# Kernel tuning notes

Hardware: AMD Instinct MI355X
Metric: run time of the kernel (lower is better)

Reference implementation:

```python
import jax, jax.numpy as jnp
import numpy as np

K = 32        # neighbors kept
SCALE = 1     # dilation stride for dilated kNN


def setup_inputs() -> dict:
    key = jax.random.key(0)
    ks = jax.random.split(key, 8)
    s = 0.05  # weight init scale
    return {
        "x": jax.random.normal(ks[0], (16, 3, 4096), jnp.float32),
        "w1": jax.random.normal(ks[1], (64, 3), jnp.float32) * s,
        "b1": jnp.zeros((64,), jnp.float32),
        "w2": jax.random.normal(ks[2], (128, 64), jnp.float32) * s,
        "b2": jnp.zeros((128,), jnp.float32),
        "w3": jax.random.normal(ks[3], (1024, 128), jnp.float32) * s,
        "b3": jnp.zeros((1024,), jnp.float32),
        "fw1": jax.random.normal(ks[4], (512, 1024), jnp.float32) * s,
        "fb1": jnp.zeros((512,), jnp.float32),
        "fw2": jax.random.normal(ks[5], (256, 512), jnp.float32) * s,
        "fb2": jnp.zeros((256,), jnp.float32),
        "fw3": jax.random.normal(ks[6], (9, 256), jnp.float32) * s,
        "fb3": jnp.zeros((9,), jnp.float32),
    }


def _knn_idx(x):
    # x: (B, C, N). Returns (B, N, K) indices of K nearest neighbors (dilated by SCALE).
    inner = jnp.einsum('bcn,bcm->bnm', x, x)            # (B, N, N)
    sq = jnp.sum(x * x, axis=1)                          # (B, N)
    neg_dist = 2.0 * inner - sq[:, :, None] - sq[:, None, :]  # = -||xi-xj||^2
    _, idx = jax.lax.top_k(neg_dist, K * SCALE)          # (B, N, K*SCALE)
    return idx[:, :, ::SCALE]                            # (B, N, K)


def reference(x, w1, b1, w2, b2, w3, b3, fw1, fb1, fw2, fb2, fw3, fb3):
    B, C, N = x.shape
    idx = _knn_idx(x)                                    # (B, N, K)
    xt = jnp.swapaxes(x, 1, 2)                           # (B, N, C)
    # gather neighbors: nbrs[b,n,k,c] = xt[b, idx[b,n,k], c]
    nbrs = jax.vmap(lambda xb, ib: xb[ib])(xt, idx)      # (B, N, K, C)
    x0 = nbrs - xt[:, :, None, :]                        # edge features x_j - x_i

    # STN (T-Net): shared MLP over edges, global max pool, FC head -> 3x3 transform
    h = jax.nn.relu(jnp.einsum('bnkc,oc->bnko', x0, w1) + b1)
    h = jax.nn.relu(jnp.einsum('bnkc,oc->bnko', h, w2) + b2)
    h = jax.nn.relu(jnp.einsum('bnkc,oc->bnko', h, w3) + b3)
    g = jnp.max(h, axis=(1, 2))                          # (B, 1024)
    f = jax.nn.relu(g @ fw1.T + fb1)
    f = jax.nn.relu(f @ fw2.T + fb2)
    t = (f @ fw3.T + fb3).reshape(B, 3, 3) + jnp.eye(3, dtype=x.dtype)

    out = jnp.einsum('bnc,bcd->bnd', xt, t)              # bmm(x^T, t)
    return jnp.swapaxes(out, 1, 2)                       # (B, 3, N)
```

## Files before the change

### kernel.cpp

```cpp
#include <hip/hip_runtime.h>
#include <hip/hip_fp8.h>

typedef __bf16 bf16_t;
typedef __bf16 bf16x8 __attribute__((ext_vector_type(8)));
typedef float floatx16 __attribute__((ext_vector_type(16)));
typedef int intx8 __attribute__((ext_vector_type(8)));
typedef unsigned long long u64;

#define B_ 16
#define N_ 4096
#define K_ 32


__device__ __forceinline__ unsigned enc_f(float f) {
    unsigned u = __float_as_uint(f);
    return (u & 0x80000000u) ? ~u : (u | 0x80000000u);
}
__device__ __forceinline__ float dec_f(unsigned e) {
    return __uint_as_float((e & 0x80000000u) ? (e & 0x7fffffffu) : ~e);
}

__device__ __forceinline__ void ce(unsigned& a, unsigned& b) {
    const unsigned mn = a < b ? a : b;
    const unsigned mx = a < b ? b : a;
    a = mn; b = mx;
}

__global__ __launch_bounds__(512, 4) void knn_kernel(
    const float* __restrict__ x, const float* __restrict__ w3,
    const float* __restrict__ w2, unsigned short* __restrict__ idxb,
    unsigned* __restrict__ g_enc, unsigned char* __restrict__ w3f8,
    bf16_t* __restrict__ w2sw)
{
    __shared__ __align__(16) float4 cand[16 * 257];
    unsigned* lists = (unsigned*)cand;
    unsigned* m1 = ((unsigned*)cand) + 8192;
    const int tid = threadIdx.x;
    const int bid = blockIdx.x;

    {
        const int g = bid * 512 + tid;
        if (g < 131072) {
            const int j  = g & 31;
            const int lI = (g >> 5) & 63;
            const int kq = (g >> 11) & 1;
            const int cb = g >> 12;
            const int mt2 = kq * 2 + (j >> 4), q = j & 15;
            const int lmI = lI & 31, hiI = lI >> 5;
            const int ch = mt2 * 32 + (q & 3) + 8 * (q >> 2) + 4 * hiI;
            __hip_fp8_e4m3 t(16.0f * w3[(cb * 32 + lmI) * 128 + ch]);
            w3f8[g] = t.__x;
        } else if (g < 139264) {
            const int o = g - 131072;
            const int f = o >> 9, r = o & 511, lI = r >> 3, jj = r & 7;
            const int ks = f & 3, nb = f >> 2, lmI = lI & 31, hiI = lI >> 5;
            w2sw[o] = (bf16_t)w2[(nb * 32 + lmI) * 64 + ks * 16 + hiI * 8 + jj];
        } else if (g < 155648) {
            g_enc[g - 139264] = 0u;
        }
    }

    const int b  = bid >> 7;
    const int q  = tid >> 4;
    const int n  = (bid & 127) * 32 + q;
    const int t  = tid & 15;
    const float* xb = x + b * 3 * N_;

    for (int j = tid; j < N_; j += 512) {
        float cx = xb[j], cy = xb[N_ + j], cz = xb[2 * N_ + j];
        cand[j + (j >> 8)] = make_float4(-2.f * cx, -2.f * cy, -2.f * cz,
                                         fmaf(cx, cx, fmaf(cy, cy, cz * cz)));
    }
    __syncthreads();

    const float xi0 = xb[n], xi1 = xb[N_ + n], xi2 = xb[2 * N_ + n];
    const float xisq1 = fmaf(xi0, xi0, fmaf(xi1, xi1, xi2 * xi2)) + 1.0f;

    unsigned r[8];
    #pragma unroll
    for (int s = 0; s < 8; s++) r[s] = 0x7F7FFFFFu;

    const int j0 = t * 256;
    const int pb = t * 257;
    #pragma unroll 1
    for (int jb = 0; jb < 256; jb += 8) {
        unsigned k[8];
        #pragma unroll
        for (int u = 0; u < 8; u++) {
            const float4 c = cand[pb + jb + u];
            const float d = fmaf(c.z, xi2, fmaf(c.y, xi1, fmaf(c.x, xi0, c.w)));
            k[u] = (__float_as_uint(d + xisq1) & 0xFFFFF000u)
                 | (unsigned)(j0 + jb + u);
        }
        ce(k[0], k[1]); ce(k[2], k[3]); ce(k[4], k[5]); ce(k[6], k[7]);
        ce(k[0], k[2]); ce(k[1], k[3]); ce(k[4], k[6]); ce(k[5], k[7]);
        ce(k[1], k[2]); ce(k[5], k[6]);
        ce(k[0], k[4]); ce(k[1], k[5]); ce(k[2], k[6]); ce(k[3], k[7]);
        ce(k[2], k[4]); ce(k[3], k[5]);
        ce(k[1], k[2]); ce(k[3], k[4]); ce(k[5], k[6]);
        unsigned s[8];
        #pragma unroll
        for (int u = 0; u < 8; u++)
            s[u] = r[u] < k[7 - u] ? r[u] : k[7 - u];
        ce(s[0], s[4]); ce(s[1], s[5]); ce(s[2], s[6]); ce(s[3], s[7]);
        ce(s[0], s[2]); ce(s[1], s[3]); ce(s[4], s[6]); ce(s[5], s[7]);
        ce(s[0], s[1]); ce(s[2], s[3]); ce(s[4], s[5]); ce(s[6], s[7]);
        #pragma unroll
        for (int u = 0; u < 8; u++) r[u] = s[u];
    }
    __syncthreads();

    #pragma unroll
    for (int k = 0; k < 8; k++) lists[tid * 9 + k] = r[k];
    __syncthreads();

    if (tid < 128) {
        const int q1 = tid >> 2, gi = tid & 3;
        const int base = (q1 * 16 + gi * 4) * 9;
        unsigned h0 = lists[base], h1 = lists[base + 9];
        unsigned h2 = lists[base + 18], h3 = lists[base + 27];
        int p0 = 0, p1 = 0, p2 = 0, p3 = 0;
        unsigned* outp = m1 + (q1 * 4 + gi) * 32;
        #pragma unroll 1
        for (int k = 0; k < 32; k++) {
            const unsigned m01 = h0 < h1 ? h0 : h1;
            const unsigned m23 = h2 < h3 ? h2 : h3;
            const unsigned v = m01 < m23 ? m01 : m23;
            outp[k] = v;
            if (m01 < m23) {
                if (h1 < h0) { p1++; h1 = p1 < 8 ? lists[base + 9 + p1] : 0xFFFFFFFFu; }
                else         { p0++; h0 = p0 < 8 ? lists[base + p0]     : 0xFFFFFFFFu; }
            } else {
                if (h3 < h2) { p3++; h3 = p3 < 8 ? lists[base + 27 + p3] : 0xFFFFFFFFu; }
                else         { p2++; h2 = p2 < 8 ? lists[base + 18 + p2] : 0xFFFFFFFFu; }
            }
        }
    }
    __syncthreads();

    if (tid < 32) {
        const unsigned* g0 = m1 + tid * 128;
        unsigned h0 = g0[0], h1 = g0[32], h2 = g0[64], h3 = g0[96];
        int p0 = 0, p1 = 0, p2 = 0, p3 = 0;
        const int nq = (bid & 127) * 32 + tid;
        unsigned short* op = idxb + ((size_t)(b * N_ + nq)) * K_;
        #pragma unroll 1
        for (int k = 0; k < K_; k++) {
            const unsigned m01 = h0 < h1 ? h0 : h1;
            const unsigned m23 = h2 < h3 ? h2 : h3;
            const unsigned v = m01 < m23 ? m01 : m23;
            op[k] = (unsigned short)(v & 0xFFFu);
            if (m01 < m23) {
                if (h1 < h0) { p1++; h1 = p1 < 32 ? g0[32 + p1] : 0xFFFFFFFFu; }
                else         { p0++; h0 = p0 < 32 ? g0[p0]      : 0xFFFFFFFFu; }
            } else {
                if (h3 < h2) { p3++; h3 = p3 < 32 ? g0[96 + p3] : 0xFFFFFFFFu; }
                else         { p2++; h2 = p2 < 32 ? g0[64 + p2] : 0xFFFFFFFFu; }
            }
        }
    }
}

__device__ __forceinline__ void chunk_epilogue(
    const floatx16& a0, const floatx16& a1, int cb, unsigned* gl, int lm)
{
    float c0 = fmaxf(a0[0], a1[0]);
    float c1 = fmaxf(a0[1], a1[1]);
    float c2 = fmaxf(a0[2], a1[2]);
    float c3 = fmaxf(a0[3], a1[3]);
    #pragma unroll
    for (int o = 4; o < 16; o += 4) {
        c0 = fmaxf(fmaxf(a0[o + 0], a1[o + 0]), c0);
        c1 = fmaxf(fmaxf(a0[o + 1], a1[o + 1]), c1);
        c2 = fmaxf(fmaxf(a0[o + 2], a1[o + 2]), c2);
        c3 = fmaxf(fmaxf(a0[o + 3], a1[o + 3]), c3);
    }
    const float m = fmaxf(fmaxf(c0, c1), fmaxf(c2, c3));
    atomicMax(&gl[cb * 32 + lm], enc_f(m));
}

__global__ __launch_bounds__(256, 3) void mlp_kernel(
    const float* __restrict__ x, const unsigned short* __restrict__ idxb,
    const float* __restrict__ w1, const float* __restrict__ b1,
    const float* __restrict__ b2,
    const bf16_t* __restrict__ w2sw, const unsigned char* __restrict__ w3f8,
    unsigned* __restrict__ g_enc)
{
    __shared__ unsigned gl[1024];
    __shared__ __align__(16) float4 w1l[64];
    __shared__ __align__(16) float b2s[128];

    const int tid = threadIdx.x;
    const int b   = blockIdx.x >> 9;
    const int p0  = (blockIdx.x & 511) * 8;
    const float* xb = x + b * 3 * N_;

    const int wv = tid >> 6;
    const int l  = tid & 63;
    const int lm = l & 31;
    const int hi = l >> 5;

    for (int i = tid; i < 1024; i += 256) gl[i] = 0u;
    if (tid < 64)
        w1l[tid] = make_float4(w1[tid * 3], w1[tid * 3 + 1], w1[tid * 3 + 2], b1[tid]);
    else if (tid < 192)
        b2s[tid - 64] = 256.0f * b2[tid - 64];
    __syncthreads();

    const unsigned char* w3p = w3f8 + l * 32;
#define PREFETCH_W3(dst, c) do {                                              \
        dst[0] = *(const intx8*)(w3p + (c) * 4096);                           \
        dst[1] = *(const intx8*)(w3p + (c) * 4096 + 2048);                    \
    } while (0)

    intx8 bwA[2], bwB[2];
    PREFETCH_W3(bwA, 0);

    bf16x8 b1h[2][4];
    float d0[2], d1[2], d2[2];
    #pragma unroll
    for (int nt2 = 0; nt2 < 2; nt2++) {
        const int pp = p0 + wv * 2 + nt2;
        const int j  = idxb[((size_t)(b * N_ + pp)) * K_ + lm];
        d0[nt2] = xb[j]          - xb[pp];
        d1[nt2] = xb[N_ + j]     - xb[N_ + pp];
        d2[nt2] = xb[2 * N_ + j] - xb[2 * N_ + pp];
    }
    #pragma unroll
    for (int ks = 0; ks < 4; ks++)
        #pragma unroll
        for (int jj = 0; jj < 8; jj++) {
            const float4 w = w1l[ks * 16 + hi * 8 + jj];
            #pragma unroll
            for (int nt2 = 0; nt2 < 2; nt2++)
                b1h[nt2][ks][jj] = (bf16_t)fmaxf(
                    fmaf(w.z, d2[nt2], fmaf(w.y, d1[nt2], fmaf(w.x, d0[nt2], w.w))), 0.f);
        }

    intx8 a3v[2][2];
    #pragma unroll
    for (int mt2 = 0; mt2 < 4; mt2++) {
        floatx16 acc0 = (floatx16)0.f, acc1 = (floatx16)0.f;
        #pragma unroll
        for (int ks = 0; ks < 4; ks++) {
            const bf16x8 aw = *(const bf16x8*)&w2sw[((mt2 * 4 + ks) * 64 + l) * 8];
            acc0 = __builtin_amdgcn_mfma_f32_32x32x16_bf16(aw, b1h[0][ks], acc0, 0, 0, 0);
            acc1 = __builtin_amdgcn_mfma_f32_32x32x16_bf16(aw, b1h[1][ks], acc1, 0, 0, 0);
        }
        const int kq = mt2 >> 1, c0 = (mt2 & 1) * 4;
        #pragma unroll
        for (int i2 = 0; i2 < 4; i2++) {
            const float4 bb = *(const float4*)&b2s[mt2 * 32 + i2 * 8 + hi * 4];
            {
                const float v0 = fmaxf(fmaf(acc0[4 * i2 + 0], 256.f, bb.x), 0.f);
                const float v1 = fmaxf(fmaf(acc0[4 * i2 + 1], 256.f, bb.y), 0.f);
                const float v2 = fmaxf(fmaf(acc0[4 * i2 + 2], 256.f, bb.z), 0.f);
                const float v3 = fmaxf(fmaf(acc0[4 * i2 + 3], 256.f, bb.w), 0.f);
                int w = __builtin_amdgcn_cvt_pk_fp8_f32(v0, v1, 0, false);
                w = __builtin_amdgcn_cvt_pk_fp8_f32(v2, v3, w, true);
                a3v[0][kq][c0 + i2] = w;
            }
            {
                const float v0 = fmaxf(fmaf(acc1[4 * i2 + 0], 256.f, bb.x), 0.f);
                const float v1 = fmaxf(fmaf(acc1[4 * i2 + 1], 256.f, bb.y), 0.f);
                const float v2 = fmaxf(fmaf(acc1[4 * i2 + 2], 256.f, bb.z), 0.f);
                const float v3 = fmaxf(fmaf(acc1[4 * i2 + 3], 256.f, bb.w), 0.f);
                int w = __builtin_amdgcn_cvt_pk_fp8_f32(v0, v1, 0, false);
                w = __builtin_amdgcn_cvt_pk_fp8_f32(v2, v3, w, true);
                a3v[1][kq][c0 + i2] = w;
            }
        }
    }

    const floatx16 zf = (floatx16)0.f;

#define COMPUTE_W3(d0_, d1_, buf) do {                                        \
        __builtin_amdgcn_s_setprio(1);                                        \
        d0_ = __builtin_amdgcn_mfma_scale_f32_32x32x64_f8f6f4(                \
            a3v[0][0], buf[0], zf, 0, 0, 0, 0x7F7F7F7F, 0, 0x7F7F7F7F);       \
        d1_ = __builtin_amdgcn_mfma_scale_f32_32x32x64_f8f6f4(                \
            a3v[1][0], buf[0], zf, 0, 0, 0, 0x7F7F7F7F, 0, 0x7F7F7F7F);       \
        d0_ = __builtin_amdgcn_mfma_scale_f32_32x32x64_f8f6f4(                \
            a3v[0][1], buf[1], d0_, 0, 0, 0, 0x7F7F7F7F, 0, 0x7F7F7F7F);      \
        d1_ = __builtin_amdgcn_mfma_scale_f32_32x32x64_f8f6f4(                \
            a3v[1][1], buf[1], d1_, 0, 0, 0, 0x7F7F7F7F, 0, 0x7F7F7F7F);      \
        __builtin_amdgcn_s_setprio(0); } while (0)

    floatx16 pA0, pA1, pB0, pB1;

    PREFETCH_W3(bwB, 1);
    COMPUTE_W3(pA0, pA1, bwA);

    #pragma unroll 1
    for (int cc = 0; cc < 15; cc++) {
        PREFETCH_W3(bwA, 2 * cc + 2);
        COMPUTE_W3(pB0, pB1, bwB);
        chunk_epilogue(pA0, pA1, 2 * cc, gl, lm);
        PREFETCH_W3(bwB, 2 * cc + 3);
        COMPUTE_W3(pA0, pA1, bwA);
        chunk_epilogue(pB0, pB1, 2 * cc + 1, gl, lm);
    }
    COMPUTE_W3(pB0, pB1, bwB);
    chunk_epilogue(pA0, pA1, 30, gl, lm);
    chunk_epilogue(pB0, pB1, 31, gl, lm);

#undef PREFETCH_W3
#undef COMPUTE_W3

    __syncthreads();
    for (int i = tid; i < 1024; i += 256)
        atomicMax(&g_enc[b * 1024 + i], gl[i]);
}

__global__ __launch_bounds__(256) void head_kernel(
    const unsigned* __restrict__ g_enc, const float* __restrict__ b3,
    const float* __restrict__ fw1, const float* __restrict__ fb1,
    const float* __restrict__ fw2, const float* __restrict__ fb2,
    const float* __restrict__ fw3, const float* __restrict__ fb3,
    float* __restrict__ tmat)
{
    __shared__ __align__(16) float g[1024];
    __shared__ __align__(16) float f1[512];
    __shared__ __align__(16) float f2[256];
    const int t = threadIdx.x, b = blockIdx.x;

    for (int i = t; i < 1024; i += 256)
        g[i] = fmaxf(fmaf(dec_f(g_enc[b * 1024 + i]), 2.44140625e-4f, b3[i]), 0.f);
    __syncthreads();

    for (int o = t; o < 512; o += 256) {
        const float4* wr = (const float4*)(fw1 + (size_t)o * 1024);
        const float4* gv = (const float4*)g;
        float acc = fb1[o];
        for (int i = 0; i < 256; i++) {
            float4 a = wr[i], c = gv[i];
            acc = fmaf(a.x, c.x, acc); acc = fmaf(a.y, c.y, acc);
            acc = fmaf(a.z, c.z, acc); acc = fmaf(a.w, c.w, acc);
        }
        f1[o] = fmaxf(acc, 0.f);
    }
    __syncthreads();
    {
        const int o = t;
        const float4* wr = (const float4*)(fw2 + (size_t)o * 512);
        const float4* fv = (const float4*)f1;
        float acc = fb2[o];
        for (int i = 0; i < 128; i++) {
            float4 a = wr[i], c = fv[i];
            acc = fmaf(a.x, c.x, acc); acc = fmaf(a.y, c.y, acc);
            acc = fmaf(a.z, c.z, acc); acc = fmaf(a.w, c.w, acc);
        }
        f2[o] = fmaxf(acc, 0.f);
    }
    __syncthreads();
    if (t < 9) {
        const float4* wr = (const float4*)(fw3 + (size_t)t * 256);
        const float4* fv = (const float4*)f2;
        float acc = fb3[t];
        for (int i = 0; i < 64; i++) {
            float4 a = wr[i], c = fv[i];
            acc = fmaf(a.x, c.x, acc); acc = fmaf(a.y, c.y, acc);
            acc = fmaf(a.z, c.z, acc); acc = fmaf(a.w, c.w, acc);
        }
        if (t == 0 || t == 4 || t == 8) acc += 1.f;
        tmat[b * 9 + t] = acc;
    }
}

__global__ __launch_bounds__(256) void out_kernel(
    const float* __restrict__ x, const float* __restrict__ tmat,
    float* __restrict__ out)
{
    const int gid = blockIdx.x * 256 + threadIdx.x;
    const int b = gid >> 12, n = gid & 4095;
    const float* T = tmat + b * 9;
    const float x0 = x[b * 12288 + n];
    const float x1 = x[b * 12288 + 4096 + n];
    const float x2 = x[b * 12288 + 8192 + n];
    #pragma unroll
    for (int d = 0; d < 3; d++)
        out[b * 12288 + d * 4096 + n] =
            fmaf(x2, T[6 + d], fmaf(x1, T[3 + d], x0 * T[d]));
}

extern "C" void kernel_launch(void* const* d_in, const int* in_sizes, int n_in,
                              void* d_out, int out_size, void* d_ws, size_t ws_size,
                              hipStream_t stream) {
    const float* x   = (const float*)d_in[0];
    const float* w1  = (const float*)d_in[1];
    const float* b1  = (const float*)d_in[2];
    const float* w2  = (const float*)d_in[3];
    const float* b2  = (const float*)d_in[4];
    const float* w3  = (const float*)d_in[5];
    const float* b3  = (const float*)d_in[6];
    const float* fw1 = (const float*)d_in[7];
    const float* fb1 = (const float*)d_in[8];
    const float* fw2 = (const float*)d_in[9];
    const float* fb2 = (const float*)d_in[10];
    const float* fw3 = (const float*)d_in[11];
    const float* fb3 = (const float*)d_in[12];
    float* out = (float*)d_out;

    char* ws = (char*)d_ws;
    unsigned short* idxb = (unsigned short*)ws;
    unsigned* g_enc = (unsigned*)(ws + 4194304);
    unsigned char* w3f8 = (unsigned char*)(ws + 4259840);
    bf16_t* w2sw = (bf16_t*)(ws + 4390912);
    float* tmat  = (float*)(ws + 4407296);

    knn_kernel<<<2048, 512, 0, stream>>>(x, w3, w2, idxb, g_enc, w3f8, w2sw);
    mlp_kernel<<<8192, 256, 0, stream>>>(x, idxb, w1, b1, b2, w2sw, w3f8, g_enc);
    head_kernel<<<16, 256, 0, stream>>>(g_enc, b3, fw1, fb1, fw2, fb2, fw3, fb3, tmat);
    out_kernel<<<256, 256, 0, stream>>>(x, tmat, out);
}
```

Before: 522.1 us.

## Split head FC1 across many blocks, compute layer-1 via MFMA, use v_max3

The head kernel's first FC layer moves into its own kernel with 128 blocks, each computing 64 outputs with a 4-way split-K reduction, instead of 16 blocks doing all 512 outputs serially. The per-edge 3->64 layer in the MLP kernel now runs as two bf16 MFMAs with the bias folded in as a constant-one input, replacing scalar FMAs, and w2 is re-swizzled to match the MFMA output layout. The max-pool epilogue uses inline v_max3_f32. This adds one kernel launch and an intermediate buffer, and rounds layer-1 inputs and weights to bf16.

Measured after the change: 465.4 us. 10.9% less time.

```diff
diff --git a/kernel.cpp b/kernel.cpp
--- a/kernel.cpp
+++ b/kernel.cpp
@@ -18,6 +18,12 @@
 }
 __device__ __forceinline__ float dec_f(unsigned e) {
     return __uint_as_float((e & 0x80000000u) ? (e & 0x7fffffffu) : ~e);
+}
+
+__device__ __forceinline__ float max3f(float a, float b, float c) {
+    float d;
+    asm("v_max3_f32 %0, %1, %2, %3" : "=v"(d) : "v"(a), "v"(b), "v"(c));
+    return d;
 }
 
 __device__ __forceinline__ void ce(unsigned& a, unsigned& b) {
@@ -54,7 +60,8 @@
             const int o = g - 131072;
             const int f = o >> 9, r = o & 511, lI = r >> 3, jj = r & 7;
             const int ks = f & 3, nb = f >> 2, lmI = lI & 31, hiI = lI >> 5;
-            w2sw[o] = (bf16_t)w2[(nb * 32 + lmI) * 64 + ks * 16 + hiI * 8 + jj];
+            const int ic = ks * 16 + 4 * hiI + 8 * (jj >> 2) + (jj & 3);
+            w2sw[o] = (bf16_t)w2[(nb * 32 + lmI) * 64 + ic];
         } else if (g < 155648) {
             g_enc[g - 139264] = 0u;
         }
@@ -170,12 +177,12 @@
     float c3 = fmaxf(a0[3], a1[3]);
     #pragma unroll
     for (int o = 4; o < 16; o += 4) {
-        c0 = fmaxf(fmaxf(a0[o + 0], a1[o + 0]), c0);
-        c1 = fmaxf(fmaxf(a0[o + 1], a1[o + 1]), c1);
-        c2 = fmaxf(fmaxf(a0[o + 2], a1[o + 2]), c2);
-        c3 = fmaxf(fmaxf(a0[o + 3], a1[o + 3]), c3);
-    }
-    const float m = fmaxf(fmaxf(c0, c1), fmaxf(c2, c3));
+        c0 = max3f(a0[o + 0], a1[o + 0], c0);
+        c1 = max3f(a0[o + 1], a1[o + 1], c1);
+        c2 = max3f(a0[o + 2], a1[o + 2], c2);
+        c3 = max3f(a0[o + 3], a1[o + 3], c3);
+    }
+    const float m = max3f(c0, c1, fmaxf(c2, c3));
     atomicMax(&gl[cb * 32 + lm], enc_f(m));
 }
 
@@ -207,6 +214,8 @@
         b2s[tid - 64] = 256.0f * b2[tid - 64];
     __syncthreads();
 
+    const floatx16 zf = (floatx16)0.f;
+
     const unsigned char* w3p = w3f8 + l * 32;
 #define PREFETCH_W3(dst, c) do {                                              \
         dst[0] = *(const intx8*)(w3p + (c) * 4096);                           \
@@ -216,7 +225,6 @@
     intx8 bwA[2], bwB[2];
     PREFETCH_W3(bwA, 0);
 
-    bf16x8 b1h[2][4];
     float d0[2], d1[2], d2[2];
     #pragma unroll
     for (int nt2 = 0; nt2 < 2; nt2++) {
@@ -226,16 +234,37 @@
         d1[nt2] = xb[N_ + j]     - xb[N_ + pp];
         d2[nt2] = xb[2 * N_ + j] - xb[2 * N_ + pp];
     }
-    #pragma unroll
-    for (int ks = 0; ks < 4; ks++)
-        #pragma unroll
-        for (int jj = 0; jj < 8; jj++) {
-            const float4 w = w1l[ks * 16 + hi * 8 + jj];
+
+    bf16x8 a1f[2];
+    #pragma unroll
+    for (int tt = 0; tt < 2; tt++) {
+        const float4 w = w1l[tt * 32 + lm];
+        bf16x8 v = (bf16x8)(bf16_t)0.f;
+        if (hi == 0) {
+            v[0] = (bf16_t)w.x; v[1] = (bf16_t)w.y;
+            v[2] = (bf16_t)w.z; v[3] = (bf16_t)w.w;
+        }
+        a1f[tt] = v;
+    }
+
+    bf16x8 b1h[2][4];
+    #pragma unroll
+    for (int nt2 = 0; nt2 < 2; nt2++) {
+        bf16x8 bf = (bf16x8)(bf16_t)0.f;
+        if (hi == 0) {
+            bf[0] = (bf16_t)d0[nt2]; bf[1] = (bf16_t)d1[nt2];
+            bf[2] = (bf16_t)d2[nt2]; bf[3] = (bf16_t)1.0f;
+        }
+        floatx16 hacc[2];
+        hacc[0] = __builtin_amdgcn_mfma_f32_32x32x16_bf16(a1f[0], bf, zf, 0, 0, 0);
+        hacc[1] = __builtin_amdgcn_mfma_f32_32x32x16_bf16(a1f[1], bf, zf, 0, 0, 0);
+        #pragma unroll
+        for (int ks = 0; ks < 4; ks++)
             #pragma unroll
-            for (int nt2 = 0; nt2 < 2; nt2++)
+            for (int jj = 0; jj < 8; jj++)
                 b1h[nt2][ks][jj] = (bf16_t)fmaxf(
-                    fmaf(w.z, d2[nt2], fmaf(w.y, d1[nt2], fmaf(w.x, d0[nt2], w.w))), 0.f);
-        }
+                    hacc[ks >> 1][(jj & 3) + 4 * (jj >> 2) + 8 * (ks & 1)], 0.f);
+    }
 
     intx8 a3v[2][2];
     #pragma unroll
@@ -272,8 +301,6 @@
         }
     }
 
-    const floatx16 zf = (floatx16)0.f;
-
 #define COMPUTE_W3(d0_, d1_, buf) do {                                        \
         __builtin_amdgcn_s_setprio(1);                                        \
         d0_ = __builtin_amdgcn_mfma_scale_f32_32x32x64_f8f6f4(                \
@@ -312,33 +339,51 @@
         atomicMax(&g_enc[b * 1024 + i], gl[i]);
 }
 
-__global__ __launch_bounds__(256) void head_kernel(
+__global__ __launch_bounds__(256) void head1_kernel(
     const unsigned* __restrict__ g_enc, const float* __restrict__ b3,
     const float* __restrict__ fw1, const float* __restrict__ fb1,
+    float* __restrict__ f1buf)
+{
+    __shared__ __align__(16) float g[1024];
+    __shared__ float red[256];
+    const int t = threadIdx.x;
+    const int b = blockIdx.x >> 3;
+    const int s = blockIdx.x & 7;
+
+    for (int i = t; i < 1024; i += 256)
+        g[i] = fmaxf(fmaf(dec_f(g_enc[b * 1024 + i]), 2.44140625e-4f, b3[i]), 0.f);
+    __syncthreads();
+
+    const int o = s * 64 + (t & 63);
+    const int quarter = t >> 6;
+    const float4* wr = (const float4*)(fw1 + (size_t)o * 1024) + quarter * 64;
+    const float4* gv = (const float4*)g + quarter * 64;
+    float acc = 0.f;
+    #pragma unroll 4
+    for (int i = 0; i < 64; i++) {
+        float4 a = wr[i], c = gv[i];
+        acc = fmaf(a.x, c.x, acc); acc = fmaf(a.y, c.y, acc);
+        acc = fmaf(a.z, c.z, acc); acc = fmaf(a.w, c.w, acc);
+    }
+    red[t] = acc;
+    __syncthreads();
+    if (t < 64) {
+        const float v = red[t] + red[t + 64] + red[t + 128] + red[t + 192];
+        f1buf[b * 512 + s * 64 + t] = fmaxf(v + fb1[s * 64 + t], 0.f);
+    }
+}
+
+__global__ __launch_bounds__(256) void head2_kernel(
+    const float* __restrict__ f1buf,
     const float* __restrict__ fw2, const float* __restrict__ fb2,
     const float* __restrict__ fw3, const float* __restrict__ fb3,
     float* __restrict__ tmat)
 {
-    __shared__ __align__(16) float g[1024];
     __shared__ __align__(16) float f1[512];
     __shared__ __align__(16) float f2[256];
     const int t = threadIdx.x, b = blockIdx.x;
 
-    for (int i = t; i < 1024; i += 256)
-        g[i] = fmaxf(fmaf(dec_f(g_enc[b * 1024 + i]), 2.44140625e-4f, b3[i]), 0.f);
-    __syncthreads();
-
-    for (int o = t; o < 512; o += 256) {
-        const float4* wr = (const float4*)(fw1 + (size_t)o * 1024);
-        const float4* gv = (const float4*)g;
-        float acc = fb1[o];
-        for (int i = 0; i < 256; i++) {
-            float4 a = wr[i], c = gv[i];
-            acc = fmaf(a.x, c.x, acc); acc = fmaf(a.y, c.y, acc);
-            acc = fmaf(a.z, c.z, acc); acc = fmaf(a.w, c.w, acc);
-        }
-        f1[o] = fmaxf(acc, 0.f);
-    }
+    if (t < 128) ((float4*)f1)[t] = ((const float4*)(f1buf + b * 512))[t];
     __syncthreads();
     {
         const int o = t;
@@ -407,9 +452,11 @@
     unsigned char* w3f8 = (unsigned char*)(ws + 4259840);
     bf16_t* w2sw = (bf16_t*)(ws + 4390912);
     float* tmat  = (float*)(ws + 4407296);
+    float* f1buf = (float*)(ws + 4407872);
 
     knn_kernel<<<2048, 512, 0, stream>>>(x, w3, w2, idxb, g_enc, w3f8, w2sw);
     mlp_kernel<<<8192, 256, 0, stream>>>(x, idxb, w1, b1, b2, w2sw, w3f8, g_enc);
-    head_kernel<<<16, 256, 0, stream>>>(g_enc, b3, fw1, fb1, fw2, fb2, fw3, fb3, tmat);
+    head1_kernel<<<128, 256, 0, stream>>>(g_enc, b3, fw1, fb1, f1buf);
+    head2_kernel<<<16, 256, 0, stream>>>(f1buf, fw2, fb2, fw3, fb3, tmat);
     out_kernel<<<256, 256, 0, stream>>>(x, tmat, out);
 }
```
